# Kernel optimization log

Measured on AMD Instinct MI355X. Metric: run time of the kernel, lower is better.

Reference implementation:

```python
import jax, jax.numpy as jnp
import numpy as np

B, S, D, H = 2, 2048, 1024, 16
DK = D // H


def setup_inputs() -> dict:
    key = jax.random.key(0)
    ks = jax.random.split(key, 12)
    s = 1.0 / np.sqrt(D)
    inp = {
        "key": jax.random.normal(ks[0], (B, S, D), jnp.float32),
        "query": jax.random.normal(ks[1], (B, S, D), jnp.float32),
        "value": jax.random.normal(ks[2], (B, S, D), jnp.float32),
        # causal mask, broadcastable to (B, H, S, S)
        "mask": jnp.tril(jnp.ones((S, S), jnp.int32))[None, None, :, :],
        "Wq": jax.random.normal(ks[3], (D, D), jnp.float32) * s,
        "bq": jax.random.normal(ks[4], (D,), jnp.float32) * s,
        "Wk": jax.random.normal(ks[5], (D, D), jnp.float32) * s,
        "bk": jax.random.normal(ks[6], (D,), jnp.float32) * s,
        "Wv": jax.random.normal(ks[7], (D, D), jnp.float32) * s,
        "bv": jax.random.normal(ks[8], (D,), jnp.float32) * s,
        "Wo": jax.random.normal(ks[9], (D, D), jnp.float32) * s,
        "bo": jax.random.normal(ks[10], (D,), jnp.float32) * s,
    }
    return inp


def reference(key, query, value, mask, Wq, bq, Wk, bk, Wv, bv, Wo, bo):
    # Linear projections (torch nn.Linear: x @ W.T + b)
    k = key @ Wk.T + bk
    q = query @ Wq.T + bq
    v = value @ Wv.T + bv
    # Faithful to source: raw view (B, H, S, DK), NO transpose --
    # this splits the SEQUENCE dim across heads, matching the original code.
    k = k.reshape(B, H, S, DK)
    q = q.reshape(B, H, S, DK)
    v = v.reshape(B, H, S, DK)
    # Scores scaled by sqrt(d_model) (as in source, not sqrt(d_k))
    scores = jnp.einsum('bhqd,bhkd->bhqk', q, k) / jnp.sqrt(jnp.float32(D))
    scores = jnp.where(mask == 0, -jnp.inf, scores)
    attn = jax.nn.softmax(scores, axis=-1)  # dropout p=0.0 -> identity
    x = jnp.einsum('bhqk,bhkd->bhqd', attn, v)
    # Faithful raw view merge: (B, H, S, DK) -> (B, S, H*DK)
    x = x.reshape(B, S, H * DK)
    return x @ Wo.T + bo
```

## Files before the change

kernel.cpp:

```cpp
#include <hip/hip_runtime.h>
#include <stdint.h>

typedef unsigned short u16;
typedef __attribute__((ext_vector_type(8))) short bfrag8;
typedef __attribute__((ext_vector_type(4))) float f32x4;
typedef __attribute__((ext_vector_type(8))) unsigned short u16x8;
typedef __attribute__((ext_vector_type(4))) unsigned short u16x4;

__device__ __forceinline__ u16 f2bf(float f) {
  union { float f; uint32_t u; } v; v.f = f;
  return (u16)((v.u + 0x7FFFu + ((v.u >> 16) & 1u)) >> 16);
}

__device__ __forceinline__ uint32_t cvtpk_bf16(float a, float b) {
  uint32_t r;
  asm("v_cvt_pk_bf16_f32 %0, %1, %2" : "=v"(r) : "v"(a), "v"(b));
  return r;
}

__device__ __forceinline__ void gload16(const void* g, void* l) {
  __builtin_amdgcn_global_load_lds(
      (const __attribute__((address_space(1))) void*)g,
      (__attribute__((address_space(3))) void*)l, 16, 0, 0);
}

struct CvtJob { const float* src; u16* dst; int n4; };
struct CvtBatch { CvtJob j[7]; };

__global__ void cvt_batch(CvtBatch b) {
  CvtJob jb = b.j[blockIdx.y];
  int i = blockIdx.x * blockDim.x + threadIdx.x;
  if (i >= jb.n4) return;
  float4 v = reinterpret_cast<const float4*>(jb.src)[i];
  u16x4 o;
  o[0] = f2bf(v.x); o[1] = f2bf(v.y); o[2] = f2bf(v.z); o[3] = f2bf(v.w);
  reinterpret_cast<u16x4*>(jb.dst)[i] = o;
}

struct Gemm3 {
  const u16* A[3];
  const u16* W[3];
  const float* bias[3];
  void* C[3];
};

template<int OUT_F32, int BM, int WM, int MINW>
__global__ __launch_bounds__(256, MINW) void gemm_nt_bias(Gemm3 g) {
  constexpr int K = 1024, N = 1024;
  constexpr int BK = 32;
  __shared__ __align__(16) u16 As[2][BM][BK];
  __shared__ __align__(16) u16 Bs[2][128][BK];
  const int z = blockIdx.z;
  const u16* __restrict__ A = g.A[z];
  const u16* __restrict__ W = g.W[z];
  const float* __restrict__ bias = g.bias[z];
  const int tid = threadIdx.x, lane = tid & 63, wave = tid >> 6;
  const int lr = lane & 15, lg = lane >> 4;
  const int wr = (wave >> 1) * (WM * 16), wc = (wave & 1) * 64;
  const int bm = blockIdx.x * BM, bn = blockIdx.y * 128;
  const int s16row = lane >> 2, s16c = (lane & 3) * 8;

  f32x4 acc[WM][4] = {};

  auto STAGE = [&](int k0, int bufi) {
    constexpr int AR = BM / 4;
    const int ar0 = wave * AR;
#pragma unroll
    for (int i = 0; i < AR / 16; i++)
      gload16(A + (size_t)(bm + ar0 + i * 16 + s16row) * K + k0 + s16c,
              &As[bufi][ar0 + i * 16][0]);
    const int br0 = wave * 32;
#pragma unroll
    for (int i = 0; i < 2; i++)
      gload16(W + (size_t)(bn + br0 + i * 16 + s16row) * K + k0 + s16c,
              &Bs[bufi][br0 + i * 16][0]);
  };

  STAGE(0, 0);
  __syncthreads();
  int buf = 0;

  for (int k0 = 0; k0 < K; k0 += BK) {
    if (k0 + BK < K) STAGE(k0 + BK, buf ^ 1);
    bfrag8 af[WM], bf[4];
#pragma unroll
    for (int mi = 0; mi < WM; mi++)
      af[mi] = *(const bfrag8*)&As[buf][wr + mi * 16 + lr][lg * 8];
#pragma unroll
    for (int ni = 0; ni < 4; ni++)
      bf[ni] = *(const bfrag8*)&Bs[buf][wc + ni * 16 + lr][lg * 8];
#pragma unroll
    for (int mi = 0; mi < WM; mi++)
#pragma unroll
      for (int ni = 0; ni < 4; ni++)
        acc[mi][ni] = __builtin_amdgcn_mfma_f32_16x16x32_bf16(af[mi], bf[ni], acc[mi][ni], 0, 0, 0);
    __syncthreads();
    buf ^= 1;
  }

  const int col0 = bn + wc + lr;
#pragma unroll
  for (int ni = 0; ni < 4; ni++) {
    int col = col0 + ni * 16;
    float bv = bias[col];
#pragma unroll
    for (int mi = 0; mi < WM; mi++) {
      int row = bm + wr + mi * 16 + lg * 4;
#pragma unroll
      for (int r = 0; r < 4; r++) {
        float v = acc[mi][ni][r] + bv;
        if (OUT_F32)
          ((float*)g.C[z])[(size_t)(row + r) * N + col] = v;
        else
          ((u16*)g.C[z])[(size_t)(row + r) * N + col] = f2bf(v);
      }
    }
  }
}

__global__ void vtrans_kernel(const u16* __restrict__ Vp, u16* __restrict__ VT,
                              unsigned* __restrict__ ctr) {
  if (blockIdx.x == 0 && blockIdx.y == 0 && threadIdx.x < 8) ctr[threadIdx.x * 16] = 0u;
  __shared__ u16 T[64][66];
  const int kt = blockIdx.x, bh = blockIdx.y;
  const int tid = threadIdx.x;
  const u16* src = Vp + (size_t)bh * 131072 + (size_t)kt * 64 * 64;
#pragma unroll
  for (int i = 0; i < 2; i++) {
    int u = tid + 256 * i;
    int row = u >> 3, c = (u & 7) * 8;
    u16x8 v = *(const u16x8*)(src + row * 64 + c);
#pragma unroll
    for (int j = 0; j < 8; j++) T[c + j][row] = v[j];
  }
  __syncthreads();
  u16* dst = VT + (size_t)bh * 131072 + (size_t)kt * 64;
#pragma unroll
  for (int i = 0; i < 2; i++) {
    int u = tid + 256 * i;
    int d = u >> 3, c = (u & 7) * 8;
    u16x8 o = *(const u16x8*)&T[d][c];
    *(u16x8*)(dst + (size_t)d * 2048 + c) = o;
  }
}

__global__ __launch_bounds__(256, 3) void attn_kernel(
    const u16* __restrict__ Qp, const u16* __restrict__ Kp,
    const u16* __restrict__ VT, u16* __restrict__ X,
    unsigned* __restrict__ ctr)
{
  __shared__ __align__(16) u16 Ks[2][64][64];
  __shared__ __align__(16) u16 Vs[2][64][64];
  constexpr int LDP = 72;
  __shared__ __align__(16) u16 Ps[4][16][LDP];
  __shared__ unsigned s_unit;

  const int tid = threadIdx.x, lane = tid & 63, w = tid >> 6;
  const int lr = lane & 15, lg = lane >> 4;
  const int grp = (int)(blockIdx.x & 7);
  unsigned* __restrict__ gctr = ctr + grp * 16;
  const int srow = lane >> 3;
  const int schunk = (lane & 7) ^ srow;
  const float C2 = 0.045084939f;
  const float THR = 11.5f;

  for (;;) {
    __syncthreads();
    if (tid == 0) s_unit = atomicAdd(gctr, 1u);
    __syncthreads();
    const unsigned u = s_unit;
    if (u >= 128u) return;
    const int j = 31 - (int)(u >> 2);
    const int bh = grp * 4 + (int)(u & 3u);
    const size_t base = (size_t)bh * 131072;
    const u16* __restrict__ Qb = Qp + base;
    const u16* __restrict__ Kb = Kp + base;
    const u16* __restrict__ Vtb = VT + base;
    const int qrow0 = j * 64 + w * 16;
    const int q = qrow0 + lr;

    bfrag8 qf[2];
#pragma unroll
    for (int ds = 0; ds < 2; ds++)
      qf[ds] = *(const bfrag8*)(Qb + (size_t)(qrow0 + lr) * 64 + ds * 32 + lg * 8);

    f32x4 oacc[4] = {};
    float m_run = -INFINITY, l_run = 0.f;

    auto STAGE = [&](int kt, int bufi) {
      const u16* gk = Kb + (size_t)(kt * 64 + w * 16 + srow) * 64 + schunk * 8;
      gload16(gk,       &Ks[bufi][w * 16][0]);
      gload16(gk + 512, &Ks[bufi][w * 16 + 8][0]);
      const u16* gv = Vtb + (size_t)(w * 16 + srow) * 2048 + kt * 64 + schunk * 8;
      gload16(gv,            &Vs[bufi][w * 16][0]);
      gload16(gv + 8 * 2048, &Vs[bufi][w * 16 + 8][0]);
    };

    STAGE(0, 0);
    __syncthreads();
    int buf = 0;

    for (int kt = 0; kt <= j; kt++) {
      if (kt < j) STAGE(kt + 1, buf ^ 1);

      f32x4 sacc[4];
#pragma unroll
      for (int kf = 0; kf < 4; kf++) sacc[kf] = (f32x4){0.f, 0.f, 0.f, 0.f};
#pragma unroll
      for (int kf = 0; kf < 4; kf++) {
        const int krow = kf * 16 + lr;
        bfrag8 kb0 = *(const bfrag8*)&Ks[buf][krow][((lg) ^ (krow & 7)) * 8];
        bfrag8 kb1 = *(const bfrag8*)&Ks[buf][krow][((lg + 4) ^ (krow & 7)) * 8];
        sacc[kf] = __builtin_amdgcn_mfma_f32_16x16x32_bf16(kb0, qf[0], sacc[kf], 0, 0, 0);
        sacc[kf] = __builtin_amdgcn_mfma_f32_16x16x32_bf16(kb1, qf[1], sacc[kf], 0, 0, 0);
      }

      if (kt == j) {
#pragma unroll
        for (int kf = 0; kf < 4; kf++)
#pragma unroll
          for (int r = 0; r < 4; r++) {
            int kg = kt * 64 + kf * 16 + lg * 4 + r;
            if (kg > q) sacc[kf][r] = -INFINITY;
          }
      }

      float a0 = fmaxf(fmaxf(sacc[0][0], sacc[0][1]), fmaxf(sacc[0][2], sacc[0][3]));
      float a1 = fmaxf(fmaxf(sacc[1][0], sacc[1][1]), fmaxf(sacc[1][2], sacc[1][3]));
      float a2 = fmaxf(fmaxf(sacc[2][0], sacc[2][1]), fmaxf(sacc[2][2], sacc[2][3]));
      float a3 = fmaxf(fmaxf(sacc[3][0], sacc[3][1]), fmaxf(sacc[3][2], sacc[3][3]));
      float smax = fmaxf(fmaxf(a0, a1), fmaxf(a2, a3));
      smax = fmaxf(smax, __shfl_xor(smax, 16));
      smax = fmaxf(smax, __shfl_xor(smax, 32));
      float pmax = smax * C2;
      float mnew = m_run;
      if (!__all(pmax <= m_run + THR)) {
        mnew = fmaxf(m_run, pmax);
        float corr = __builtin_amdgcn_exp2f(m_run - mnew);
        l_run *= corr;
#pragma unroll
        for (int df = 0; df < 4; df++)
#pragma unroll
          for (int r = 0; r < 4; r++) oacc[df][r] *= corr;
        m_run = mnew;
      }

      float rs = 0.f;
#pragma unroll
      for (int kf = 0; kf < 4; kf++) {
        float p0 = __builtin_amdgcn_exp2f(__builtin_fmaf(sacc[kf][0], C2, -mnew));
        float p1 = __builtin_amdgcn_exp2f(__builtin_fmaf(sacc[kf][1], C2, -mnew));
        float p2 = __builtin_amdgcn_exp2f(__builtin_fmaf(sacc[kf][2], C2, -mnew));
        float p3 = __builtin_amdgcn_exp2f(__builtin_fmaf(sacc[kf][3], C2, -mnew));
        rs += (p0 + p1) + (p2 + p3);
        uint2 pk;
        pk.x = cvtpk_bf16(p0, p1);
        pk.y = cvtpk_bf16(p2, p3);
        *(uint2*)&Ps[w][lr][kf * 16 + lg * 4] = pk;
      }
      rs += __shfl_xor(rs, 16);
      rs += __shfl_xor(rs, 32);
      l_run += rs;

#pragma unroll
      for (int ks = 0; ks < 2; ks++) {
        bfrag8 pa = *(const bfrag8*)&Ps[w][lr][ks * 32 + lg * 8];
#pragma unroll
        for (int df = 0; df < 4; df++) {
          const int vrow = df * 16 + lr;
          bfrag8 vf = *(const bfrag8*)&Vs[buf][vrow][((ks * 4 + lg) ^ (vrow & 7)) * 8];
          oacc[df] = __builtin_amdgcn_mfma_f32_16x16x32_bf16(vf, pa, oacc[df], 0, 0, 0);
        }
      }

      __syncthreads();
      buf ^= 1;
    }

    float inv = 1.0f / l_run;
#pragma unroll
    for (int df = 0; df < 4; df++) {
      u16x4 o;
#pragma unroll
      for (int r = 0; r < 4; r++) o[r] = f2bf(oacc[df][r] * inv);
      *(u16x4*)&X[base + (size_t)q * 64 + df * 16 + lg * 4] = o;
    }
  }
}

extern "C" void kernel_launch(void* const* d_in, const int* in_sizes, int n_in,
                              void* d_out, int out_size, void* d_ws, size_t ws_size,
                              hipStream_t stream) {
  const float* key   = (const float*)d_in[0];
  const float* query = (const float*)d_in[1];
  const float* value = (const float*)d_in[2];
  const float* Wq = (const float*)d_in[4];
  const float* bq = (const float*)d_in[5];
  const float* Wk = (const float*)d_in[6];
  const float* bk = (const float*)d_in[7];
  const float* Wv = (const float*)d_in[8];
  const float* bv = (const float*)d_in[9];
  const float* Wo = (const float*)d_in[10];
  const float* bo = (const float*)d_in[11];

  u16* ws = (u16*)d_ws;
  const size_t MD = 4096ull * 1024ull;
  u16* qb  = ws;
  u16* kb  = ws + MD;
  u16* vbf = ws + 2 * MD;
  u16* Qp  = ws + 3 * MD;
  u16* Kp  = ws + 4 * MD;
  u16* Vp  = ws + 5 * MD;
  u16* Xb  = ws + 6 * MD;
  u16* wqb = ws + 7 * MD;
  u16* wkb = wqb + 1024 * 1024;
  u16* wvb = wkb + 1024 * 1024;
  u16* wob = wvb + 1024 * 1024;

  CvtBatch cb;
  cb.j[0] = { query, qb, 1048576 };
  cb.j[1] = { key,   kb, 1048576 };
  cb.j[2] = { value, vbf, 1048576 };
  cb.j[3] = { Wq, wqb, 262144 };
  cb.j[4] = { Wk, wkb, 262144 };
  cb.j[5] = { Wv, wvb, 262144 };
  cb.j[6] = { Wo, wob, 262144 };
  cvt_batch<<<dim3(4096, 7), 256, 0, stream>>>(cb);

  Gemm3 g1;
  g1.A[0] = qb;  g1.A[1] = kb;  g1.A[2] = vbf;
  g1.W[0] = wqb; g1.W[1] = wkb; g1.W[2] = wvb;
  g1.bias[0] = bq; g1.bias[1] = bk; g1.bias[2] = bv;
  g1.C[0] = Qp; g1.C[1] = Kp; g1.C[2] = Vp;
  gemm_nt_bias<0, 128, 4, 3><<<dim3(32, 8, 3), 256, 0, stream>>>(g1);

  u16* VT = vbf;
  unsigned* ctr = (unsigned*)qb;
  vtrans_kernel<<<dim3(32, 32), 256, 0, stream>>>(Vp, VT, ctr);

  attn_kernel<<<768, 256, 0, stream>>>(Qp, Kp, VT, Xb, ctr);

  Gemm3 g2;
  g2.A[0] = Xb; g2.W[0] = wob; g2.bias[0] = bo; g2.C[0] = d_out;
  g2.A[1] = g2.A[2] = nullptr; g2.W[1] = g2.W[2] = nullptr;
  g2.bias[1] = g2.bias[2] = nullptr; g2.C[1] = g2.C[2] = nullptr;
  gemm_nt_bias<1, 64, 2, 2><<<dim3(64, 8, 1), 256, 0, stream>>>(g2);
}
```

Before: 126.5 us.

## Widen GEMM K-tile to 64 with XOR-swizzled LDS and retile blocks

The projection GEMMs now stage 64-wide K slices instead of 32, halving the number of loop iterations and barriers. LDS rows are XOR-swizzled by chunk so the fragment reads avoid bank conflicts. Block tiles are changed to 128x64 for both the QKV and output GEMMs, which doubles the grid in N and unifies the configuration. The output GEMM moves from 64x128 to 128x64 tiles with higher occupancy hints. Larger LDS per block may limit occupancy.

Result: faster. 123.5 us (-2.4%).

```diff
diff --git a/kernel.cpp b/kernel.cpp
--- a/kernel.cpp
+++ b/kernel.cpp
@@ -44,36 +44,37 @@
   void* C[3];
 };
 
-template<int OUT_F32, int BM, int WM, int MINW>
+template<int OUT_F32, int BM, int BN, int MINW>
 __global__ __launch_bounds__(256, MINW) void gemm_nt_bias(Gemm3 g) {
   constexpr int K = 1024, N = 1024;
-  constexpr int BK = 32;
+  constexpr int BK = 64;
+  constexpr int WM = BM / 32, WN = BN / 32;
   __shared__ __align__(16) u16 As[2][BM][BK];
-  __shared__ __align__(16) u16 Bs[2][128][BK];
+  __shared__ __align__(16) u16 Bs[2][BN][BK];
   const int z = blockIdx.z;
   const u16* __restrict__ A = g.A[z];
   const u16* __restrict__ W = g.W[z];
   const float* __restrict__ bias = g.bias[z];
   const int tid = threadIdx.x, lane = tid & 63, wave = tid >> 6;
   const int lr = lane & 15, lg = lane >> 4;
-  const int wr = (wave >> 1) * (WM * 16), wc = (wave & 1) * 64;
-  const int bm = blockIdx.x * BM, bn = blockIdx.y * 128;
-  const int s16row = lane >> 2, s16c = (lane & 3) * 8;
-
-  f32x4 acc[WM][4] = {};
+  const int wr = (wave >> 1) * (WM * 16), wc = (wave & 1) * (WN * 16);
+  const int bm = blockIdx.x * BM, bn = blockIdx.y * BN;
+  const int srow = lane >> 3;
+  const int schunk = (lane & 7) ^ srow;
+
+  f32x4 acc[WM][WN] = {};
 
   auto STAGE = [&](int k0, int bufi) {
-    constexpr int AR = BM / 4;
-    const int ar0 = wave * AR;
-#pragma unroll
-    for (int i = 0; i < AR / 16; i++)
-      gload16(A + (size_t)(bm + ar0 + i * 16 + s16row) * K + k0 + s16c,
-              &As[bufi][ar0 + i * 16][0]);
-    const int br0 = wave * 32;
-#pragma unroll
-    for (int i = 0; i < 2; i++)
-      gload16(W + (size_t)(bn + br0 + i * 16 + s16row) * K + k0 + s16c,
-              &Bs[bufi][br0 + i * 16][0]);
+#pragma unroll
+    for (int i = 0; i < BM / 32; i++) {
+      int r = wave * (BM / 4) + i * 8;
+      gload16(A + (size_t)(bm + r + srow) * K + k0 + schunk * 8, &As[bufi][r][0]);
+    }
+#pragma unroll
+    for (int i = 0; i < BN / 32; i++) {
+      int r = wave * (BN / 4) + i * 8;
+      gload16(W + (size_t)(bn + r + srow) * K + k0 + schunk * 8, &Bs[bufi][r][0]);
+    }
   };
 
   STAGE(0, 0);
@@ -82,25 +83,34 @@
 
   for (int k0 = 0; k0 < K; k0 += BK) {
     if (k0 + BK < K) STAGE(k0 + BK, buf ^ 1);
-    bfrag8 af[WM], bf[4];
-#pragma unroll
-    for (int mi = 0; mi < WM; mi++)
-      af[mi] = *(const bfrag8*)&As[buf][wr + mi * 16 + lr][lg * 8];
-#pragma unroll
-    for (int ni = 0; ni < 4; ni++)
-      bf[ni] = *(const bfrag8*)&Bs[buf][wc + ni * 16 + lr][lg * 8];
-#pragma unroll
-    for (int mi = 0; mi < WM; mi++)
-#pragma unroll
-      for (int ni = 0; ni < 4; ni++)
-        acc[mi][ni] = __builtin_amdgcn_mfma_f32_16x16x32_bf16(af[mi], bf[ni], acc[mi][ni], 0, 0, 0);
+    bfrag8 af[2][WM], bf[2][WN];
+#pragma unroll
+    for (int ks = 0; ks < 2; ks++) {
+#pragma unroll
+      for (int mi = 0; mi < WM; mi++) {
+        const int row = wr + mi * 16 + lr;
+        af[ks][mi] = *(const bfrag8*)&As[buf][row][((ks * 4 + lg) ^ (row & 7)) * 8];
+      }
+#pragma unroll
+      for (int ni = 0; ni < WN; ni++) {
+        const int row = wc + ni * 16 + lr;
+        bf[ks][ni] = *(const bfrag8*)&Bs[buf][row][((ks * 4 + lg) ^ (row & 7)) * 8];
+      }
+    }
+#pragma unroll
+    for (int ks = 0; ks < 2; ks++)
+#pragma unroll
+      for (int mi = 0; mi < WM; mi++)
+#pragma unroll
+        for (int ni = 0; ni < WN; ni++)
+          acc[mi][ni] = __builtin_amdgcn_mfma_f32_16x16x32_bf16(af[ks][mi], bf[ks][ni], acc[mi][ni], 0, 0, 0);
     __syncthreads();
     buf ^= 1;
   }
 
   const int col0 = bn + wc + lr;
 #pragma unroll
-  for (int ni = 0; ni < 4; ni++) {
+  for (int ni = 0; ni < WN; ni++) {
     int col = col0 + ni * 16;
     float bv = bias[col];
 #pragma unroll
@@ -332,7 +342,7 @@
   g1.W[0] = wqb; g1.W[1] = wkb; g1.W[2] = wvb;
   g1.bias[0] = bq; g1.bias[1] = bk; g1.bias[2] = bv;
   g1.C[0] = Qp; g1.C[1] = Kp; g1.C[2] = Vp;
-  gemm_nt_bias<0, 128, 4, 3><<<dim3(32, 8, 3), 256, 0, stream>>>(g1);
+  gemm_nt_bias<0, 128, 64, 3><<<dim3(32, 16, 3), 256, 0, stream>>>(g1);
 
   u16* VT = vbf;
   unsigned* ctr = (unsigned*)qb;
@@ -344,5 +354,5 @@
   g2.A[0] = Xb; g2.W[0] = wob; g2.bias[0] = bo; g2.C[0] = d_out;
   g2.A[1] = g2.A[2] = nullptr; g2.W[1] = g2.W[2] = nullptr;
   g2.bias[1] = g2.bias[2] = nullptr; g2.C[1] = g2.C[2] = nullptr;
-  gemm_nt_bias<1, 64, 2, 2><<<dim3(64, 8, 1), 256, 0, stream>>>(g2);
-}
+  gemm_nt_bias<1, 128, 64, 3><<<dim3(32, 16, 1), 256, 0, stream>>>(g2);
+}
```
